# Kernel optimization log

Measured on AMD Instinct MI355X. Metric: run time of the kernel, lower is better.

The kernel has to match this reference:

```python
import jax, jax.numpy as jnp
import numpy as np

N = 20000
IN_CH, HID, OUT_CH = 512, 64, 16
H1, H2 = 8, 1
NEG_SLOPE = 0.2


def setup_inputs() -> dict:
    key = jax.random.key(0)
    ks = jax.random.split(key, 10)
    E = 320000
    x = jax.random.normal(ks[0], (N, IN_CH), dtype=jnp.float32)
    edge_index = jax.random.randint(ks[1], (2, E), 0, N, dtype=jnp.int64)
    s = 0.05
    return {
        "x": x,
        "edge_index": edge_index,
        "W1": jax.random.normal(ks[2], (H1 * HID, IN_CH), dtype=jnp.float32) * s,
        "att_src1": jax.random.normal(ks[3], (1, H1, HID), dtype=jnp.float32) * s,
        "att_dst1": jax.random.normal(ks[4], (1, H1, HID), dtype=jnp.float32) * s,
        "b1": jnp.zeros((H1 * HID,), dtype=jnp.float32),
        "W2": jax.random.normal(ks[5], (H2 * OUT_CH, H1 * HID), dtype=jnp.float32) * s,
        "att_src2": jax.random.normal(ks[6], (1, H2, OUT_CH), dtype=jnp.float32) * s,
        "att_dst2": jax.random.normal(ks[7], (1, H2, OUT_CH), dtype=jnp.float32) * s,
        "b2": jnp.zeros((OUT_CH,), dtype=jnp.float32),
    }


def _gat_conv(x, src, dst, W, att_src, att_dst, bias, heads, out_ch, concat):
    # Linear transform: [N, H, C]
    h = (x @ W.T).reshape(x.shape[0], heads, out_ch)
    n = x.shape[0]
    # Per-node attention logits (a_src . h), (a_dst . h): [N, H]
    a_s = (h * att_src).sum(-1)
    a_d = (h * att_dst).sum(-1)
    # Edge-wise LeakyReLU attention: [E, H]
    e = a_s[src] + a_d[dst]
    e = jnp.where(e >= 0, e, NEG_SLOPE * e)
    # Segment softmax over incoming edges of each destination node
    m = jax.ops.segment_max(e, dst, num_segments=n)
    p = jnp.exp(e - m[dst])
    z = jax.ops.segment_sum(p, dst, num_segments=n)
    alpha = p / z[dst]  # [E, H]
    # Weighted scatter-aggregate: out[dst] += alpha * h[src]
    msg = h[src] * alpha[:, :, None]  # [E, H, C]
    out = jax.ops.segment_sum(msg, dst, num_segments=n)
    out = out.reshape(n, heads * out_ch) if concat else out.mean(axis=1)
    return out + bias


def reference(x, edge_index, W1, att_src1, att_dst1, b1, W2, att_src2, att_dst2, b2):
    # PyG GATConv adds self-loops by default
    loops = jnp.arange(N, dtype=edge_index.dtype)
    src = jnp.concatenate([edge_index[0], loops])
    dst = jnp.concatenate([edge_index[1], loops])
    # dropout layers are identity in eval mode
    h = _gat_conv(x, src, dst, W1, att_src1, att_dst1, b1, H1, HID, True)
    h = jax.nn.relu(h)
    out = _gat_conv(h, src, dst, W2, att_src2, att_dst2, b2, H2, OUT_CH, False)
    return out
```

## Files before the change

kernel.cpp:

```cpp
#include <hip/hip_runtime.h>

#define Nn     20000
#define IN_CH  512
#define C1     512
#define H1n    8
#define HIDn   64
#define OUT_CH 16
#define En     320000
#define EPn    340000
#define NEG    0.2f

typedef __attribute__((ext_vector_type(8))) short bf16x8;
typedef __attribute__((ext_vector_type(4))) float f32x4;

__device__ inline unsigned short bf16_rne(float f) {
  unsigned int u = __float_as_uint(f);
  return (unsigned short)((u + 0x7fffu + ((u >> 16) & 1u)) >> 16);
}
__device__ inline float bf16_f(unsigned short u) {
  return __uint_as_float(((unsigned int)u) << 16);
}

#define NX8  (Nn * IN_CH / 8)
#define NW8  (C1 * IN_CH / 8)
#define NW28 (OUT_CH * C1 / 8)
#define NZ4  (2 * Nn / 4)
__global__ __launch_bounds__(256) void cvt3_kernel(
    const float* __restrict__ x,  unsigned short* __restrict__ xb,
    const float* __restrict__ W1, unsigned short* __restrict__ w1b,
    const float* __restrict__ W2, unsigned short* __restrict__ w2b,
    int* __restrict__ zbase)
{
  int i = blockIdx.x * 256 + threadIdx.x;
  const float* in; unsigned short* ob; int idx;
  if (i < NX8) { in = x; ob = xb; idx = i; }
  else if (i < NX8 + NW8) { in = W1; ob = w1b; idx = i - NX8; }
  else if (i < NX8 + NW8 + NW28) { in = W2; ob = w2b; idx = i - NX8 - NW8; }
  else if (i < NX8 + NW8 + NW28 + NZ4) {
    int4 zz = {0, 0, 0, 0};
    ((int4*)zbase)[i - NX8 - NW8 - NW28] = zz;
    return;
  } else return;
  float4 f0 = ((const float4*)in)[idx * 2];
  float4 f1 = ((const float4*)in)[idx * 2 + 1];
  float f[8] = {f0.x, f0.y, f0.z, f0.w, f1.x, f1.y, f1.z, f1.w};
  unsigned short h[8];
#pragma unroll
  for (int j = 0; j < 8; j++) h[j] = bf16_rne(f[j]);
  ushort4 hv0 = {h[0], h[1], h[2], h[3]}, hv1 = {h[4], h[5], h[6], h[7]};
  ((ushort4*)ob)[idx * 2] = hv0; ((ushort4*)ob)[idx * 2 + 1] = hv1;
}

#define GLL(gp, lp) __builtin_amdgcn_global_load_lds( \
    (const __attribute__((address_space(1))) void*)(gp), \
    (__attribute__((address_space(3))) void*)(lp), 16, 0, 0)

#define SWZ(c) ((c) ^ (((c) >> 3) & 3))

__global__ __launch_bounds__(256, 3) void gemm1_mfma(
    const unsigned short* __restrict__ Ab, const unsigned short* __restrict__ Bb,
    const float* __restrict__ attS, const float* __restrict__ attD,
    unsigned short* __restrict__ Cb, float* __restrict__ as1, float* __restrict__ ad1)
{
  __shared__ unsigned short sA[128 * 32], sB[128 * 32];
  int t = threadIdx.x;
  int wgid = blockIdx.x;
  int bm = (wgid & 7) + 8 * (wgid >> 5);
  int bn = (wgid >> 3) & 3;
  if (bm >= 157) return;
  int lane = t & 63, w = t >> 6;

  int slot0 = w * 128 + lane;
  int slot1 = slot0 + 64;
  int cb0 = w * 128, cb1 = w * 128 + 64;
  int cs0 = SWZ(slot0), cs1 = SWZ(slot1);
  int ar0 = bm * 128 + (cs0 >> 2); if (ar0 > Nn - 1) ar0 = Nn - 1;
  int ar1 = bm * 128 + (cs1 >> 2); if (ar1 > Nn - 1) ar1 = Nn - 1;
  int br0 = bn * 128 + (cs0 >> 2);
  int br1 = bn * 128 + (cs1 >> 2);
  size_t offA0 = (size_t)ar0 * IN_CH + (cs0 & 3) * 8;
  size_t offA1 = (size_t)ar1 * IN_CH + (cs1 & 3) * 8;
  size_t offB0 = (size_t)br0 * IN_CH + (cs0 & 3) * 8;
  size_t offB1 = (size_t)br1 * IN_CH + (cs1 & 3) * 8;

  int wm = (w >> 1) * 64, wn = (w & 1) * 64;
  int lr = lane & 15, kb = lane >> 4;

  f32x4 acc[4][4] = {};

  for (int k0 = 0; k0 < IN_CH; k0 += 32) {
    __syncthreads();
    GLL(Ab + offA0 + k0, sA + cb0 * 8);
    GLL(Ab + offA1 + k0, sA + cb1 * 8);
    GLL(Bb + offB0 + k0, sB + cb0 * 8);
    GLL(Bb + offB1 + k0, sB + cb1 * 8);
    __syncthreads();

    bf16x8 ah[4], bh[4];
#pragma unroll
    for (int i = 0; i < 4; i++) {
      int rca = (wm + i * 16 + lr) * 4 + kb;
      ah[i] = *(const bf16x8*)&sA[SWZ(rca) * 8];
      int rcb = (wn + i * 16 + lr) * 4 + kb;
      bh[i] = *(const bf16x8*)&sB[SWZ(rcb) * 8];
    }
#pragma unroll
    for (int i = 0; i < 4; i++)
#pragma unroll
      for (int j = 0; j < 4; j++)
        acc[i][j] = __builtin_amdgcn_mfma_f32_16x16x32_bf16(ah[i], bh[j], acc[i][j], 0, 0, 0);
  }

  int lq = lane >> 4;
#pragma unroll
  for (int i = 0; i < 4; i++) {
    int r0 = bm * 128 + wm + i * 16 + lq * 4;
#pragma unroll
    for (int j = 0; j < 4; j++) {
      int ccol = bn * 128 + wn + j * 16 + lr;
#pragma unroll
      for (int q = 0; q < 4; q++) {
        unsigned int myv = bf16_rne(acc[i][j][q]);
        unsigned int pv = __shfl_xor(myv, 1);
        int r = r0 + q;
        if (!(lr & 1) && r < Nn) {
          unsigned int word = myv | (pv << 16);
          *(unsigned int*)&Cb[(size_t)r * C1 + ccol] = word;
        }
      }
    }
  }
  int hh = bn * 2 + (wn >> 6);
  float aSj[4], aDj[4];
#pragma unroll
  for (int j = 0; j < 4; j++) {
    int cc = bn * 128 + wn + j * 16 + lr;
    aSj[j] = attS[cc]; aDj[j] = attD[cc];
  }
#pragma unroll
  for (int i = 0; i < 4; i++)
#pragma unroll
    for (int q = 0; q < 4; q++) {
      float s = acc[i][0][q] * aSj[0] + acc[i][1][q] * aSj[1]
              + acc[i][2][q] * aSj[2] + acc[i][3][q] * aSj[3];
      float dd = acc[i][0][q] * aDj[0] + acc[i][1][q] * aDj[1]
               + acc[i][2][q] * aDj[2] + acc[i][3][q] * aDj[3];
#pragma unroll
      for (int off = 1; off < 16; off <<= 1) {
        s += __shfl_xor(s, off);
        dd += __shfl_xor(dd, off);
      }
      int r = bm * 128 + wm + i * 16 + lq * 4 + q;
      if (lr == 0 && r < Nn) { as1[r * 8 + hh] = s; ad1[r * 8 + hh] = dd; }
    }
}

__global__ void hist_kernel(const int* __restrict__ ei, int* __restrict__ cnt)
{
  int e4 = (blockIdx.x * 256 + threadIdx.x) * 4;
  if (e4 >= EPn) return;
  if (e4 < En) {
    int4 dv = *(const int4*)&ei[En + e4];
    atomicAdd(&cnt[dv.x], 1); atomicAdd(&cnt[dv.y], 1);
    atomicAdd(&cnt[dv.z], 1); atomicAdd(&cnt[dv.w], 1);
  } else {
    int d = e4 - En;
    atomicAdd(&cnt[d], 1);     atomicAdd(&cnt[d + 1], 1);
    atomicAdd(&cnt[d + 2], 1); atomicAdd(&cnt[d + 3], 1);
  }
}

__global__ __launch_bounds__(1024) void scan_kernel(
    const int* __restrict__ cnt, int* __restrict__ row)
{
  __shared__ int wsum[16];
  int t = threadIdx.x;
  int base = t * 20;
  int v[20];
  int s = 0;
#pragma unroll
  for (int j = 0; j < 20; j++) {
    int i = base + j;
    int c = (i < Nn) ? cnt[i] : 0;
    v[j] = s;
    s += c;
  }
  int lane = t & 63, w = t >> 6;
  int incl = s;
#pragma unroll
  for (int off = 1; off < 64; off <<= 1) {
    int o = __shfl_up(incl, off);
    if (lane >= off) incl += o;
  }
  if (lane == 63) wsum[w] = incl;
  __syncthreads();
  if (w == 0) {
    int ws = (lane < 16) ? wsum[lane] : 0;
#pragma unroll
    for (int off = 1; off < 16; off <<= 1) {
      int o = __shfl_up(ws, off);
      if (lane >= off) ws += o;
    }
    if (lane < 16) wsum[lane] = ws;
  }
  __syncthreads();
  int excl = ((w > 0) ? wsum[w - 1] : 0) + incl - s;
#pragma unroll
  for (int j = 0; j < 20; j++) {
    int i = base + j;
    if (i < Nn) row[i] = excl + v[j];
  }
  if (t == 0) row[Nn] = EPn;
}

__global__ void scatter_kernel(const int* __restrict__ ei, const int* __restrict__ row,
                               int* __restrict__ cur, int* __restrict__ csr)
{
  int e4 = (blockIdx.x * 256 + threadIdx.x) * 4;
  if (e4 >= EPn) return;
  if (e4 < En) {
    int4 sv = *(const int4*)&ei[e4];
    int4 dv = *(const int4*)&ei[En + e4];
    int sa[4] = {sv.x, sv.y, sv.z, sv.w};
    int da[4] = {dv.x, dv.y, dv.z, dv.w};
#pragma unroll
    for (int j = 0; j < 4; j++) {
      int pos = row[da[j]] + atomicAdd(&cur[da[j]], 1);
      csr[pos] = sa[j];
    }
  } else {
#pragma unroll
    for (int j = 0; j < 4; j++) {
      int d = e4 - En + j;
      int pos = row[d] + atomicAdd(&cur[d], 1);
      csr[pos] = d;
    }
  }
}

__global__ __launch_bounds__(256, 6) void agg1_kernel(
    const int* __restrict__ row, const int* __restrict__ csr,
    const unsigned short* __restrict__ h1b, const float* __restrict__ as1,
    const float* __restrict__ adv, const float* __restrict__ b1,
    const unsigned short* __restrict__ W2b,
    const float* __restrict__ attS2, const float* __restrict__ attD2,
    float* __restrict__ h2, float* __restrict__ as2, float* __restrict__ ad2)
{
  __shared__ float part[2][64 * 9];

  int t = threadIdx.x, lane = t & 63, w = t >> 6;
  int pr = w >> 1;
  int p  = w & 1;
  int d = blockIdx.x * 2 + pr;
  int beg = row[d], end = row[d + 1];
  int deg = end - beg;
  int hq = lane >> 3;
  size_t chb = (size_t)8 * lane;
  float adH = adv[d * 8 + hq];

  float a0 = 0.f, a1 = 0.f, a2 = 0.f, a3 = 0.f;
  float a4 = 0.f, a5 = 0.f, a6 = 0.f, a7 = 0.f;
  float z = 0.f;
  int nj = (deg - p + 1) >> 1;
#pragma unroll 4
  for (int j = 0; j < nj; j++) {
    int e = beg + p + 2 * j;
    int s = csr[e];
    float v = as1[s * 8 + hq] + adH;
    v = (v >= 0.f) ? v : NEG * v;
    float pp = __expf(v);
    z += pp;
    uint4 u = *(const uint4*)&h1b[(size_t)s * C1 + chb];
    a0 = fmaf(pp, __uint_as_float(u.x << 16), a0);
    a1 = fmaf(pp, __uint_as_float(u.x & 0xffff0000u), a1);
    a2 = fmaf(pp, __uint_as_float(u.y << 16), a2);
    a3 = fmaf(pp, __uint_as_float(u.y & 0xffff0000u), a3);
    a4 = fmaf(pp, __uint_as_float(u.z << 16), a4);
    a5 = fmaf(pp, __uint_as_float(u.z & 0xffff0000u), a5);
    a6 = fmaf(pp, __uint_as_float(u.w << 16), a6);
    a7 = fmaf(pp, __uint_as_float(u.w & 0xffff0000u), a7);
  }

  if (p == 1) {
    float* ps = &part[pr][lane * 9];
    ps[0] = a0; ps[1] = a1; ps[2] = a2; ps[3] = a3;
    ps[4] = a4; ps[5] = a5; ps[6] = a6; ps[7] = a7; ps[8] = z;
  }
  __syncthreads();
  if (p == 0) {
    const float* ps = &part[pr][lane * 9];
    a0 += ps[0]; a1 += ps[1]; a2 += ps[2]; a3 += ps[3];
    a4 += ps[4]; a5 += ps[5]; a6 += ps[6]; a7 += ps[7]; z += ps[8];
    float rz = 1.f / z;
    float4 b0 = *(const float4*)&b1[chb];
    float4 b4 = *(const float4*)&b1[chb + 4];
    float o0 = fmaf(a0, rz, b0.x); o0 = o0 > 0.f ? o0 : 0.f;
    float o1 = fmaf(a1, rz, b0.y); o1 = o1 > 0.f ? o1 : 0.f;
    float o2 = fmaf(a2, rz, b0.z); o2 = o2 > 0.f ? o2 : 0.f;
    float o3 = fmaf(a3, rz, b0.w); o3 = o3 > 0.f ? o3 : 0.f;
    float o4 = fmaf(a4, rz, b4.x); o4 = o4 > 0.f ? o4 : 0.f;
    float o5 = fmaf(a5, rz, b4.y); o5 = o5 > 0.f ? o5 : 0.f;
    float o6 = fmaf(a6, rz, b4.z); o6 = o6 > 0.f ? o6 : 0.f;
    float o7 = fmaf(a7, rz, b4.w); o7 = o7 > 0.f ? o7 : 0.f;

    float myh2 = 0.f, s2 = 0.f, d2 = 0.f;
#pragma unroll
    for (int j = 0; j < OUT_CH; j++) {
      bf16x8 wv = *(const bf16x8*)&W2b[j * 512 + chb];
      float pj = o0 * bf16_f((unsigned short)wv[0]) + o1 * bf16_f((unsigned short)wv[1])
               + o2 * bf16_f((unsigned short)wv[2]) + o3 * bf16_f((unsigned short)wv[3])
               + o4 * bf16_f((unsigned short)wv[4]) + o5 * bf16_f((unsigned short)wv[5])
               + o6 * bf16_f((unsigned short)wv[6]) + o7 * bf16_f((unsigned short)wv[7]);
#pragma unroll
      for (int off = 1; off < 64; off <<= 1) pj += __shfl_xor(pj, off);
      if (lane == j) myh2 = pj;
      s2 = fmaf(pj, attS2[j], s2);
      d2 = fmaf(pj, attD2[j], d2);
    }
    if (lane < OUT_CH) h2[(size_t)d * OUT_CH + lane] = myh2;
    if (lane == 0) { as2[d] = s2; ad2[d] = d2; }
  }
}

__global__ __launch_bounds__(256) void agg2_kernel(
    const int* __restrict__ row, const int* __restrict__ csr,
    const float* __restrict__ h2, const float* __restrict__ as2,
    const float* __restrict__ ad2, const float* __restrict__ b2,
    float* __restrict__ out)
{
  int wave = threadIdx.x >> 6, lane = threadIdx.x & 63;
  int d = blockIdx.x * 4 + wave;
  int beg = row[d], end = row[d + 1];
  float add = ad2[d];

  int c = lane & 15;
  float acc = 0.f, z = 0.f;
  for (int e = beg + (lane >> 4); e < end; e += 4) {
    int s = csr[e];
    float v = as2[s] + add;
    v = (v >= 0.f) ? v : NEG * v;
    float p = __expf(v);
    z += p;
    acc = fmaf(p, h2[(size_t)s * 16 + c], acc);
  }
  acc += __shfl_xor(acc, 16);
  acc += __shfl_xor(acc, 32);
  z += __shfl_xor(z, 16);
  z += __shfl_xor(z, 32);
  if (lane < 16) out[(size_t)d * 16 + lane] = acc / z + b2[lane];
}

extern "C" void kernel_launch(void* const* d_in, const int* in_sizes, int n_in,
                              void* d_out, int out_size, void* d_ws, size_t ws_size,
                              hipStream_t stream)
{
  const float* x    = (const float*)d_in[0];
  const int*   ei   = (const int*)d_in[1];
  const float* W1   = (const float*)d_in[2];
  const float* asv1 = (const float*)d_in[3];
  const float* adv1 = (const float*)d_in[4];
  const float* b1   = (const float*)d_in[5];
  const float* W2   = (const float*)d_in[6];
  const float* asv2 = (const float*)d_in[7];
  const float* adv2 = (const float*)d_in[8];
  const float* b2   = (const float*)d_in[9];
  float* out = (float*)d_out;

  unsigned short* x_b = (unsigned short*)d_ws;
  unsigned short* h1b = x_b + (size_t)Nn * IN_CH;
  unsigned short* w_b = h1b + (size_t)Nn * C1;
  unsigned short* w2b = w_b + (size_t)C1 * IN_CH;
  float* as1   = (float*)(w2b + (size_t)OUT_CH * C1);
  float* ad1   = as1 + (size_t)Nn * H1n;
  float* h2    = ad1 + (size_t)Nn * H1n;
  float* as2   = h2 + (size_t)Nn * OUT_CH;
  float* ad2   = as2 + Nn;
  int* csr  = (int*)(ad2 + Nn);
  int* cnt  = csr + EPn;
  int* cur  = cnt + Nn;
  int* rowp = cur + Nn;

  cvt3_kernel<<<(NX8 + NW8 + NW28 + NZ4 + 255) / 256, 256, 0, stream>>>(
      x, x_b, W1, w_b, W2, w2b, cnt);

  gemm1_mfma<<<640, 256, 0, stream>>>(x_b, w_b, asv1, adv1, h1b, as1, ad1);

  hist_kernel<<<(EPn / 4 + 255) / 256, 256, 0, stream>>>(ei, cnt);
  scan_kernel<<<1, 1024, 0, stream>>>(cnt, rowp);
  scatter_kernel<<<(EPn / 4 + 255) / 256, 256, 0, stream>>>(ei, rowp, cur, csr);
  agg1_kernel<<<Nn / 2, 256, 0, stream>>>(rowp, csr, h1b, as1, ad1, b1,
                                          w2b, asv2, adv2, h2, as2, ad2);
  agg2_kernel<<<Nn / 4, 256, 0, stream>>>(rowp, csr, h2, as2, ad2, b2, out);
}
```

Before: 151.1 us.

## Load fp32 x directly in GEMM and convert in-register, fuse histogram into weight convert

After: 150.5 us. No clear change (-0.3%).

```diff
diff --git a/kernel.cpp b/kernel.cpp
--- a/kernel.cpp
+++ b/kernel.cpp
@@ -21,24 +21,40 @@
   return __uint_as_float(((unsigned int)u) << 16);
 }
 
-#define NX8  (Nn * IN_CH / 8)
+__device__ inline bf16x8 pack8(float4 f0, float4 f1) {
+  unsigned int r0, r1, r2, r3;
+  asm("v_cvt_pk_bf16_f32 %0, %1, %2" : "=v"(r0) : "v"(f0.x), "v"(f0.y));
+  asm("v_cvt_pk_bf16_f32 %0, %1, %2" : "=v"(r1) : "v"(f0.z), "v"(f0.w));
+  asm("v_cvt_pk_bf16_f32 %0, %1, %2" : "=v"(r2) : "v"(f1.x), "v"(f1.y));
+  asm("v_cvt_pk_bf16_f32 %0, %1, %2" : "=v"(r3) : "v"(f1.z), "v"(f1.w));
+  union { unsigned int u[4]; bf16x8 v; } un;
+  un.u[0] = r0; un.u[1] = r1; un.u[2] = r2; un.u[3] = r3;
+  return un.v;
+}
+
 #define NW8  (C1 * IN_CH / 8)
 #define NW28 (OUT_CH * C1 / 8)
-#define NZ4  (2 * Nn / 4)
-__global__ __launch_bounds__(256) void cvt3_kernel(
-    const float* __restrict__ x,  unsigned short* __restrict__ xb,
+#define NH4  (EPn / 4)
+__global__ __launch_bounds__(256) void cvtwh_kernel(
     const float* __restrict__ W1, unsigned short* __restrict__ w1b,
     const float* __restrict__ W2, unsigned short* __restrict__ w2b,
-    int* __restrict__ zbase)
+    const int* __restrict__ ei, int* __restrict__ cnt)
 {
   int i = blockIdx.x * 256 + threadIdx.x;
   const float* in; unsigned short* ob; int idx;
-  if (i < NX8) { in = x; ob = xb; idx = i; }
-  else if (i < NX8 + NW8) { in = W1; ob = w1b; idx = i - NX8; }
-  else if (i < NX8 + NW8 + NW28) { in = W2; ob = w2b; idx = i - NX8 - NW8; }
-  else if (i < NX8 + NW8 + NW28 + NZ4) {
-    int4 zz = {0, 0, 0, 0};
-    ((int4*)zbase)[i - NX8 - NW8 - NW28] = zz;
+  if (i < NW8) { in = W1; ob = w1b; idx = i; }
+  else if (i < NW8 + NW28) { in = W2; ob = w2b; idx = i - NW8; }
+  else if (i < NW8 + NW28 + NH4) {
+    int e4 = (i - NW8 - NW28) * 4;
+    if (e4 < En) {
+      int4 dv = *(const int4*)&ei[En + e4];
+      atomicAdd(&cnt[dv.x], 1); atomicAdd(&cnt[dv.y], 1);
+      atomicAdd(&cnt[dv.z], 1); atomicAdd(&cnt[dv.w], 1);
+    } else {
+      int d = e4 - En;
+      atomicAdd(&cnt[d], 1);     atomicAdd(&cnt[d + 1], 1);
+      atomicAdd(&cnt[d + 2], 1); atomicAdd(&cnt[d + 3], 1);
+    }
     return;
   } else return;
   float4 f0 = ((const float4*)in)[idx * 2];
@@ -55,14 +71,16 @@
     (const __attribute__((address_space(1))) void*)(gp), \
     (__attribute__((address_space(3))) void*)(lp), 16, 0, 0)
 
-#define SWZ(c) ((c) ^ (((c) >> 3) & 3))
+#define SWZ(c)  ((c) ^ (((c) >> 3) & 3))
+#define SWZA(c) ((c) ^ (((c) >> 3) & 7))
 
 __global__ __launch_bounds__(256, 3) void gemm1_mfma(
-    const unsigned short* __restrict__ Ab, const unsigned short* __restrict__ Bb,
+    const float* __restrict__ Af, const unsigned short* __restrict__ Bb,
     const float* __restrict__ attS, const float* __restrict__ attD,
     unsigned short* __restrict__ Cb, float* __restrict__ as1, float* __restrict__ ad1)
 {
-  __shared__ unsigned short sA[128 * 32], sB[128 * 32];
+  __shared__ float sAf[128 * 32];
+  __shared__ unsigned short sB[128 * 32];
   int t = threadIdx.x;
   int wgid = blockIdx.x;
   int bm = (wgid & 7) + 8 * (wgid >> 5);
@@ -70,16 +88,20 @@
   if (bm >= 157) return;
   int lane = t & 63, w = t >> 6;
 
-  int slot0 = w * 128 + lane;
-  int slot1 = slot0 + 64;
-  int cb0 = w * 128, cb1 = w * 128 + 64;
+  int acb[4]; size_t aoff[4];
+#pragma unroll
+  for (int q = 0; q < 4; q++) {
+    int slot = w * 256 + q * 64 + lane;
+    acb[q] = w * 256 + q * 64;
+    int cs = SWZA(slot);
+    int ra = bm * 128 + (cs >> 3); if (ra > Nn - 1) ra = Nn - 1;
+    aoff[q] = (size_t)ra * IN_CH + (cs & 7) * 4;
+  }
+  int slot0 = w * 128 + lane, slot1 = slot0 + 64;
+  int bcb0 = w * 128, bcb1 = w * 128 + 64;
   int cs0 = SWZ(slot0), cs1 = SWZ(slot1);
-  int ar0 = bm * 128 + (cs0 >> 2); if (ar0 > Nn - 1) ar0 = Nn - 1;
-  int ar1 = bm * 128 + (cs1 >> 2); if (ar1 > Nn - 1) ar1 = Nn - 1;
   int br0 = bn * 128 + (cs0 >> 2);
   int br1 = bn * 128 + (cs1 >> 2);
-  size_t offA0 = (size_t)ar0 * IN_CH + (cs0 & 3) * 8;
-  size_t offA1 = (size_t)ar1 * IN_CH + (cs1 & 3) * 8;
   size_t offB0 = (size_t)br0 * IN_CH + (cs0 & 3) * 8;
   size_t offB1 = (size_t)br1 * IN_CH + (cs1 & 3) * 8;
 
@@ -90,17 +112,21 @@
 
   for (int k0 = 0; k0 < IN_CH; k0 += 32) {
     __syncthreads();
-    GLL(Ab + offA0 + k0, sA + cb0 * 8);
-    GLL(Ab + offA1 + k0, sA + cb1 * 8);
-    GLL(Bb + offB0 + k0, sB + cb0 * 8);
-    GLL(Bb + offB1 + k0, sB + cb1 * 8);
+    GLL(Af + aoff[0] + k0, sAf + acb[0] * 4);
+    GLL(Af + aoff[1] + k0, sAf + acb[1] * 4);
+    GLL(Af + aoff[2] + k0, sAf + acb[2] * 4);
+    GLL(Af + aoff[3] + k0, sAf + acb[3] * 4);
+    GLL(Bb + offB0 + k0, sB + bcb0 * 8);
+    GLL(Bb + offB1 + k0, sB + bcb1 * 8);
     __syncthreads();
 
     bf16x8 ah[4], bh[4];
 #pragma unroll
     for (int i = 0; i < 4; i++) {
-      int rca = (wm + i * 16 + lr) * 4 + kb;
-      ah[i] = *(const bf16x8*)&sA[SWZ(rca) * 8];
+      int c0 = (wm + i * 16 + lr) * 8 + kb * 2;
+      float4 f0 = *(const float4*)&sAf[SWZA(c0) * 4];
+      float4 f1 = *(const float4*)&sAf[SWZA(c0 + 1) * 4];
+      ah[i] = pack8(f0, f1);
       int rcb = (wn + i * 16 + lr) * 4 + kb;
       bh[i] = *(const bf16x8*)&sB[SWZ(rcb) * 8];
     }
@@ -153,21 +179,6 @@
       int r = bm * 128 + wm + i * 16 + lq * 4 + q;
       if (lr == 0 && r < Nn) { as1[r * 8 + hh] = s; ad1[r * 8 + hh] = dd; }
     }
-}
-
-__global__ void hist_kernel(const int* __restrict__ ei, int* __restrict__ cnt)
-{
-  int e4 = (blockIdx.x * 256 + threadIdx.x) * 4;
-  if (e4 >= EPn) return;
-  if (e4 < En) {
-    int4 dv = *(const int4*)&ei[En + e4];
-    atomicAdd(&cnt[dv.x], 1); atomicAdd(&cnt[dv.y], 1);
-    atomicAdd(&cnt[dv.z], 1); atomicAdd(&cnt[dv.w], 1);
-  } else {
-    int d = e4 - En;
-    atomicAdd(&cnt[d], 1);     atomicAdd(&cnt[d + 1], 1);
-    atomicAdd(&cnt[d + 2], 1); atomicAdd(&cnt[d + 3], 1);
-  }
 }
 
 __global__ __launch_bounds__(1024) void scan_kernel(
@@ -366,8 +377,7 @@
   const float* b2   = (const float*)d_in[9];
   float* out = (float*)d_out;
 
-  unsigned short* x_b = (unsigned short*)d_ws;
-  unsigned short* h1b = x_b + (size_t)Nn * IN_CH;
+  unsigned short* h1b = (unsigned short*)d_ws;
   unsigned short* w_b = h1b + (size_t)Nn * C1;
   unsigned short* w2b = w_b + (size_t)C1 * IN_CH;
   float* as1   = (float*)(w2b + (size_t)OUT_CH * C1);
@@ -380,12 +390,13 @@
   int* cur  = cnt + Nn;
   int* rowp = cur + Nn;
 
-  cvt3_kernel<<<(NX8 + NW8 + NW28 + NZ4 + 255) / 256, 256, 0, stream>>>(
-      x, x_b, W1, w_b, W2, w2b, cnt);
-
-  gemm1_mfma<<<640, 256, 0, stream>>>(x_b, w_b, asv1, adv1, h1b, as1, ad1);
-
-  hist_kernel<<<(EPn / 4 + 255) / 256, 256, 0, stream>>>(ei, cnt);
+  hipMemsetAsync(cnt, 0, 2 * Nn * sizeof(int), stream);
+
+  cvtwh_kernel<<<(NW8 + NW28 + NH4 + 255) / 256, 256, 0, stream>>>(
+      W1, w_b, W2, w2b, ei, cnt);
+
+  gemm1_mfma<<<640, 256, 0, stream>>>(x, w_b, asv1, adv1, h1b, as1, ad1);
+
   scan_kernel<<<1, 1024, 0, stream>>>(cnt, rowp);
   scatter_kernel<<<(EPn / 4 + 255) / 256, 256, 0, stream>>>(ei, rowp, cur, csr);
   agg1_kernel<<<Nn / 2, 256, 0, stream>>>(rowp, csr, h1b, as1, ad1, b1,
```
